# Kernel optimization log

Measured on AMD Instinct MI355X. Metric: run time of the kernel, lower is better.

## Reference

```python
import jax, jax.numpy as jnp
import numpy as np

DIM = 64
NUM_GRAPHS = 512


def setup_inputs() -> dict:
    key = jax.random.key(0)
    ks = jax.random.split(key, 24)
    N, E, F = 20000, 60000, 11
    rn = lambda k, s, sc: jax.random.normal(k, s, jnp.float32) * sc
    return {
        "x": jax.random.normal(ks[0], (N, F), jnp.float32),
        "edge_index": jax.random.randint(ks[1], (2, E), 0, N),
        "edge_attr": jax.random.uniform(ks[2], (E, 5), jnp.float32),
        "batch": jnp.sort(jax.random.randint(ks[3], (N,), 0, NUM_GRAPHS)),
        # lin0: num_features -> dim
        "lin0_w": rn(ks[4], (DIM, F), 0.3), "lin0_b": jnp.zeros(DIM, jnp.float32),
        # edge MLP: 5 -> 128 -> dim*dim
        "nn1_w": rn(ks[5], (128, 5), 0.3), "nn1_b": jnp.zeros(128, jnp.float32),
        "nn2_w": rn(ks[6], (DIM * DIM, 128), 0.02), "nn2_b": jnp.zeros(DIM * DIM, jnp.float32),
        # NNConv root weight + bias
        "root_w": rn(ks[7], (DIM, DIM), 0.1), "conv_b": jnp.zeros(DIM, jnp.float32),
        # GRU (input dim, hidden dim) gates r,z,n
        "gru_w_ih": rn(ks[8], (3 * DIM, DIM), 0.1), "gru_w_hh": rn(ks[9], (3 * DIM, DIM), 0.1),
        "gru_b_ih": jnp.zeros(3 * DIM, jnp.float32), "gru_b_hh": jnp.zeros(3 * DIM, jnp.float32),
        # Set2Set LSTM: input 2*dim, hidden dim, gates i,f,g,o
        "lstm_w_ih": rn(ks[10], (4 * DIM, 2 * DIM), 0.1), "lstm_w_hh": rn(ks[11], (4 * DIM, DIM), 0.1),
        "lstm_b_ih": jnp.zeros(4 * DIM, jnp.float32), "lstm_b_hh": jnp.zeros(4 * DIM, jnp.float32),
        # readout
        "lin1_w": rn(ks[12], (DIM, 2 * DIM), 0.1), "lin1_b": jnp.zeros(DIM, jnp.float32),
        "lin2_w": rn(ks[13], (1, DIM), 0.1), "lin2_b": jnp.zeros(1, jnp.float32),
    }


def reference(x, edge_index, edge_attr, batch,
              lin0_w, lin0_b, nn1_w, nn1_b, nn2_w, nn2_b, root_w, conv_b,
              gru_w_ih, gru_w_hh, gru_b_ih, gru_b_hh,
              lstm_w_ih, lstm_w_hh, lstm_b_ih, lstm_b_hh,
              lin1_w, lin1_b, lin2_w, lin2_b):
    N = x.shape[0]
    src, dst = edge_index[0], edge_index[1]
    # per-edge weight matrices from edge MLP (edge_attr is constant across the 3 conv calls)
    We = (jax.nn.relu(edge_attr @ nn1_w.T + nn1_b) @ nn2_w.T + nn2_b).reshape(-1, DIM, DIM)
    deg = jnp.maximum(jax.ops.segment_sum(jnp.ones_like(src, jnp.float32), dst, N), 1.0)[:, None]

    out = jax.nn.relu(x @ lin0_w.T + lin0_b)
    h = out  # GRU hidden, shape [N, dim]
    for _ in range(3):
        # NNConv: gather src -> per-edge matmul -> scatter-mean at dst, plus root + bias
        msg = jnp.einsum('ei,eio->eo', out[src], We)
        agg = jax.ops.segment_sum(msg, dst, N) / deg
        m = jax.nn.relu(agg + out @ root_w.T + conv_b)
        # single GRU step (PyTorch gate layout r,z,n)
        gi = m @ gru_w_ih.T + gru_b_ih
        gh = h @ gru_w_hh.T + gru_b_hh
        ir, iz, inn = jnp.split(gi, 3, -1)
        hr, hz, hn = jnp.split(gh, 3, -1)
        r = jax.nn.sigmoid(ir + hr)
        z = jax.nn.sigmoid(iz + hz)
        n = jnp.tanh(inn + r * hn)
        h = (1.0 - z) * n + z * h
        out = h

    # Set2Set pooling, 3 processing steps
    B = NUM_GRAPHS
    q_star = jnp.zeros((B, 2 * DIM), out.dtype)
    hs = jnp.zeros((B, DIM), out.dtype)
    cs = jnp.zeros((B, DIM), out.dtype)
    for _ in range(3):
        gates = q_star @ lstm_w_ih.T + lstm_b_ih + hs @ lstm_w_hh.T + lstm_b_hh
        gi, gf, gg, go = jnp.split(gates, 4, -1)
        cs = jax.nn.sigmoid(gf) * cs + jax.nn.sigmoid(gi) * jnp.tanh(gg)
        hs = jax.nn.sigmoid(go) * jnp.tanh(cs)
        q = hs
        e = jnp.sum(out * q[batch], axis=-1)                 # [N]
        emax = jax.ops.segment_max(e, batch, B)
        a = jnp.exp(e - emax[batch])
        a = a / jax.ops.segment_sum(a, batch, B)[batch]      # scatter-softmax
        r_ = jax.ops.segment_sum(a[:, None] * out, batch, B)  # [B, dim]
        q_star = jnp.concatenate([q, r_], axis=-1)

    y = jax.nn.relu(q_star @ lin1_w.T + lin1_b) @ lin2_w.T + lin2_b
    return y.reshape(-1)
```

## Files before the change

### kernel.cpp

```cpp
#include <hip/hip_runtime.h>
#include <math.h>


typedef _Float16 f16x8 __attribute__((ext_vector_type(8)));
typedef _Float16 h2 __attribute__((ext_vector_type(2)));
typedef float f32x4 __attribute__((ext_vector_type(4)));

#define BFRAG_TOTAL (66 * 4 * 4 * 64 * 8)
#define GFRAG_TOTAL (4 * 16 * 64 * 8)
#define PAIRS_CAP 40064
#define PMAX 152
#define SPLITK 4
#define ITERS 8
#define NB_BS 66
#define NB_GS 16
#define NB_H1 (PAIRS_CAP / 128)

#if __has_builtin(__builtin_amdgcn_fdot2)
#define FDOT2(a, b, c) __builtin_amdgcn_fdot2((a), (b), (c), false)
#else
__device__ __forceinline__ float FDOT2(h2 a, h2 b, float c) {
  return c + (float)a[0] * (float)b[0] + (float)a[1] * (float)b[1];
}
#endif

__global__ void k_gc(const int* __restrict__ batch, int* __restrict__ gptr,
                     const int* __restrict__ eidx, int* __restrict__ cnt,
                     int N, int E, int B) {
  int i = blockIdx.x * 256 + threadIdx.x;
  if (i < N) {
    int b = batch[i];
    int bp = (i == 0) ? -1 : batch[i - 1];
    for (int g = bp + 1; g <= b; ++g) gptr[g] = i;
    if (i == N - 1) {
      for (int g = b + 1; g <= B; ++g) gptr[g] = N;
    }
  }
  if (i < E) atomicAdd(&cnt[eidx[E + i]], 1);
}

__global__ __launch_bounds__(1024) void k_scan(const int* __restrict__ cnt,
                                               int* __restrict__ dptr2, int N) {
  __shared__ int wsum[16];
  int t = threadIdx.x;
  int lane = t & 63, wid = t >> 6;
  if (t == 0) dptr2[0] = 0;
  int running = 0;
  for (int base = 0; base < N; base += 1024) {
    int x = (base + t < N) ? ((cnt[base + t] + 1) & ~1) : 0;
#pragma unroll
    for (int d = 1; d < 64; d <<= 1) {
      int u = __shfl_up(x, d, 64);
      if (lane >= d) x += u;
    }
    if (lane == 63) wsum[wid] = x;
    __syncthreads();
    if (wid == 0) {
      int y = (lane < 16) ? wsum[lane] : 0;
#pragma unroll
      for (int d = 1; d < 16; d <<= 1) {
        int u = __shfl_up(y, d, 64);
        if (lane >= d) y += u;
      }
      if (lane < 16) wsum[lane] = y;
    }
    __syncthreads();
    int add = running + (wid > 0 ? wsum[wid - 1] : 0);
    if (base + t < N) dptr2[base + t + 1] = add + x;
    running += wsum[15];
    __syncthreads();
  }
}

__global__ void k_fill(const int* __restrict__ eidx, const int* __restrict__ dptr2,
                       int* __restrict__ fill, int* __restrict__ srcs_s,
                       int* __restrict__ eord, int E) {
  int e = blockIdx.x * 256 + threadIdx.x;
  if (e >= E) return;
  int d = eidx[E + e];
  int pos = dptr2[d] + atomicAdd(&fill[d], 1);
  srcs_s[pos] = eidx[e];
  eord[pos] = e;
}

__global__ __launch_bounds__(256) void k_prep(
    const float* __restrict__ nn2_w, const float* __restrict__ nn2_b,
    const float* __restrict__ root_w, _Float16* __restrict__ Bh,
    _Float16* __restrict__ Bl,
    const float* __restrict__ gw_ih, const float* __restrict__ gw_hh,
    _Float16* __restrict__ Gh, _Float16* __restrict__ Gl,
    const float* __restrict__ eattr, const int* __restrict__ eord,
    const int* __restrict__ eidx, const int* __restrict__ cnt,
    const float* __restrict__ nn1_w, const float* __restrict__ nn1_b,
    f16x8* __restrict__ hp, int E,
    const float* __restrict__ x, const float* __restrict__ lin0_w,
    const float* __restrict__ lin0_b, float* __restrict__ outn, int N) {
  __shared__ float shmem[8192];
  const int bid = blockIdx.x;
  const int t = threadIdx.x;

  if (bid < NB_BS) {
    float* lds = shmem;
    const int kc = bid;
    if (kc < 64) {
      for (int r = t; r < 4096; r += 256) {
        float2 v = *(const float2*)&nn2_w[(size_t)r * 128 + kc * 2];
        lds[r * 2] = v.x;
        lds[r * 2 + 1] = v.y;
      }
    } else if (kc == 64) {
      for (int r = t; r < 4096; r += 256) {
        lds[r * 2] = nn2_b[r];
        lds[r * 2 + 1] = 0.f;
      }
    } else {
      for (int r = t; r < 4096; r += 256) {
        int i = r >> 6, o = r & 63;
        lds[r * 2] = root_w[o * 64 + i];
        lds[r * 2 + 1] = 0.f;
      }
    }
    __syncthreads();
    for (int slot = t; slot < 1024; slot += 256) {
      int lane = slot & 63, c = (slot >> 6) & 3, w = slot >> 8;
      f16x8 ph, pl;
#pragma unroll
      for (int j = 0; j < 8; ++j) {
        int mm = w * 32 + ((lane >> 4) << 3) + j;
        int o = c * 16 + (lane & 15);
        int i = mm & 63, kl = mm >> 6;
        float v = lds[(i * 64 + o) * 2 + kl];
        _Float16 h = (_Float16)v;
        ph[j] = h;
        pl[j] = (_Float16)(v - (float)h);
      }
      size_t base = (((size_t)kc * 4 + w) * 4 + c) * 512 + (size_t)lane * 8;
      *(f16x8*)&Bh[base] = ph;
      *(f16x8*)&Bl[base] = pl;
    }
  } else if (bid < NB_BS + NB_GS) {
    const int c = bid - NB_BS;
    const int w = t >> 6, lane = t & 63;
    const int part = c >> 2, dblk = c & 3;
    f16x8 oh, ol;
#pragma unroll
    for (int j = 0; j < 8; ++j) {
      int k = w * 32 + ((lane >> 4) << 3) + j;
      int d = dblk * 16 + (lane & 15);
      float v;
      if (part == 0) {
        v = (k < 64) ? gw_ih[(size_t)d * 64 + k]
                     : gw_hh[(size_t)d * 64 + (k - 64)];
      } else if (part == 1) {
        v = (k < 64) ? gw_ih[(size_t)(64 + d) * 64 + k]
                     : gw_hh[(size_t)(64 + d) * 64 + (k - 64)];
      } else if (part == 2) {
        v = (k < 64) ? gw_ih[(size_t)(128 + d) * 64 + k] : 0.f;
      } else {
        v = (k >= 64) ? gw_hh[(size_t)(128 + d) * 64 + (k - 64)] : 0.f;
      }
      _Float16 h = (_Float16)v;
      oh[j] = h;
      ol[j] = (_Float16)(v - (float)h);
    }
    size_t base = ((size_t)(w * 16 + c) * 64 + lane) * 8;
    *(f16x8*)&Gh[base] = oh;
    *(f16x8*)&Gl[base] = ol;
  } else if (bid < NB_BS + NB_GS + NB_H1) {
    float* w5 = shmem;
    float* bb = shmem + 640;
    float* at = shmem + 768;
    float* idg = shmem + 2048;
    float* vf1 = shmem + 2176;
    const int m0 = (bid - NB_BS - NB_GS) * 128;
    for (int idx = t; idx < 640; idx += 256) w5[idx] = nn1_w[idx];
    if (t < 128) bb[t] = nn1_b[t];
    if (t < 128) {
      int m = m0 + t;
      int e0 = eord[2 * m], e1 = eord[2 * m + 1];
      float iv = 0.f, vf = 0.f;
      if (e0 >= 0) {
        const float* a = eattr + (size_t)e0 * 5;
#pragma unroll
        for (int q = 0; q < 5; ++q) at[t * 10 + q] = a[q];
        int dg = cnt[eidx[E + e0]];
        iv = 1.f / (float)(dg > 1 ? dg : 1);
        if (e1 >= 0) {
          const float* b = eattr + (size_t)e1 * 5;
#pragma unroll
          for (int q = 0; q < 5; ++q) at[t * 10 + 5 + q] = b[q];
          vf = 1.f;
        } else {
#pragma unroll
          for (int q = 0; q < 5; ++q) at[t * 10 + 5 + q] = 0.f;
        }
      } else {
#pragma unroll
        for (int q = 0; q < 10; ++q) at[t * 10 + q] = 0.f;
      }
      idg[t] = iv;
      vf1[t] = vf;
    }
    __syncthreads();
    const int pl = t & 127, jh = (t >> 7) * 64;
    const int m = m0 + pl;
    float a0 = at[pl * 10 + 0], a1 = at[pl * 10 + 1], a2 = at[pl * 10 + 2],
          a3 = at[pl * 10 + 3], a4 = at[pl * 10 + 4];
    float b0 = at[pl * 10 + 5], b1 = at[pl * 10 + 6], b2 = at[pl * 10 + 7],
          b3 = at[pl * 10 + 8], b4 = at[pl * 10 + 9];
    float iv = idg[pl], vf = vf1[pl];
#pragma unroll 4
    for (int ci = 0; ci < 16; ++ci) {
      int j0 = jh + ci * 4;
      f16x8 o;
#pragma unroll
      for (int u = 0; u < 4; ++u) {
        const float* wr = &w5[(j0 + u) * 5];
        float v0 = fmaxf(bb[j0 + u] + a0 * wr[0] + a1 * wr[1] + a2 * wr[2] +
                             a3 * wr[3] + a4 * wr[4], 0.f) * iv;
        float v1 = fmaxf(bb[j0 + u] + b0 * wr[0] + b1 * wr[1] + b2 * wr[2] +
                             b3 * wr[3] + b4 * wr[4], 0.f) * iv * vf;
        o[2 * u] = (_Float16)v0;
        o[2 * u + 1] = (_Float16)v1;
      }
      hp[(size_t)(j0 >> 2) * PAIRS_CAP + m] = o;
    }
  } else {
    int gid = (bid - NB_BS - NB_GS - NB_H1) * 256 + t;
    int n = gid >> 6, d = gid & 63;
    if (n >= N) return;
    const float* xr = x + (size_t)n * 11;
    const float* wr = lin0_w + d * 11;
    float acc = lin0_b[d];
#pragma unroll
    for (int f = 0; f < 11; ++f) acc += xr[f] * wr[f];
    outn[(size_t)n * 64 + d] = fmaxf(acc, 0.f);
  }
}

__global__ __launch_bounds__(512, 4) void k_fused(
    const float* __restrict__ outn, const f16x8* __restrict__ hp,
    const int* __restrict__ dptr2, const int* __restrict__ cnt,
    const int* __restrict__ srcs_s, const _Float16* __restrict__ Bh,
    const _Float16* __restrict__ Bl, float* __restrict__ agg2, int N) {
  __shared__ __align__(16) _Float16 Ah[32 * 64 * 8];
  __shared__ uint4 sbufq[PMAX * 17];
  __shared__ uint4 hpq[2][PMAX];

  const int t = threadIdx.x;
  const int w = t >> 6, lane = t & 63;
  const int wq = w & 3;
  const int c_off = (w >> 2) * 2;
  const int nl = t >> 3;
  const int io = t & 7;
  const int split = blockIdx.y;
  const int n0 = blockIdx.x * 64;
  const int n = n0 + nl;
  const bool nvalid = (n < N);
  const int hi_n = (n0 + 64 > N) ? N : (n0 + 64);
  const int p0b = dptr2[n0];
  const int p1b = dptr2[hi_n];
  const int MP0 = p0b >> 1;
  const int MPn = (p1b - p0b) >> 1;
  const bool useLds = (MPn <= PMAX);
  int mp0 = 0, mp1 = 0, deg = 0;
  if (nvalid) { mp0 = dptr2[n] >> 1; mp1 = dptr2[n + 1] >> 1; deg = cnt[n]; }
  const float inv = 1.f / (float)(deg > 1 ? deg : 1);
  const int odd = deg & 1;
  const int rt_b = nl >> 4, nm = nl & 15;
  const int MPs = useLds ? MPn : 0;

  for (int idx = t; idx < MPs * 16; idx += 512) {
    int ml = idx >> 4, g = idx & 15;
    int e0s = srcs_s[2 * (MP0 + ml)];
    int e1s = srcs_s[2 * (MP0 + ml) + 1];
    float4 r0 = *(const float4*)(outn + (size_t)e0s * 64 + g * 4);
    float4 r1 = *(const float4*)(outn + (size_t)e1s * 64 + g * 4);
    f16x8 o;
    o[0] = (_Float16)r0.x; o[1] = (_Float16)r1.x;
    o[2] = (_Float16)r0.y; o[3] = (_Float16)r1.y;
    o[4] = (_Float16)r0.z; o[5] = (_Float16)r1.z;
    o[6] = (_Float16)r0.w; o[7] = (_Float16)r1.w;
    sbufq[ml * 17 + (((g >> 2) ^ (ml & 3)) << 2) + (g & 3)] =
        __builtin_bit_cast(uint4, o);
  }
  for (int idx = t; idx < MPs; idx += 512)
    hpq[0][idx] =
        *(const uint4*)&hp[(size_t)(split * ITERS) * PAIRS_CAP + MP0 + idx];
  __syncthreads();

  f32x4 acc[4][2];
#pragma unroll
  for (int a = 0; a < 4; ++a)
#pragma unroll
    for (int c = 0; c < 2; ++c) acc[a][c] = (f32x4)(0.f);

  const int niter = (split == 0) ? (ITERS + 1) : ITERS;
  int cur = 0;
  for (int cc = 0; cc < niter; ++cc) {
    const bool extra = (cc == ITERS);

    float av[4][8];
#pragma unroll
    for (int kl = 0; kl < 4; ++kl)
#pragma unroll
      for (int j = 0; j < 8; ++j) av[kl][j] = 0.f;

    if (!extra) {
      if (useLds) {
        for (int m = mp0; m < mp1; ++m) {
          int ml = m - MP0;
          uint4 hu = hpq[cur][ml];
          h2 h0 = __builtin_bit_cast(h2, hu.x);
          h2 h1 = __builtin_bit_cast(h2, hu.y);
          h2 hh2 = __builtin_bit_cast(h2, hu.z);
          h2 h3 = __builtin_bit_cast(h2, hu.w);
          int sb = ml * 17 + (((io >> 1) ^ (ml & 3)) << 2) + (io & 1) * 2;
          uint4 su0 = sbufq[sb], su1 = sbufq[sb + 1];
          unsigned vs[8] = {su0.x, su0.y, su0.z, su0.w,
                            su1.x, su1.y, su1.z, su1.w};
#pragma unroll
          for (int v = 0; v < 8; ++v) {
            h2 sp = __builtin_bit_cast(h2, vs[v]);
            av[0][v] = FDOT2(h0, sp, av[0][v]);
            av[1][v] = FDOT2(h1, sp, av[1][v]);
            av[2][v] = FDOT2(hh2, sp, av[2][v]);
            av[3][v] = FDOT2(h3, sp, av[3][v]);
          }
        }
      } else {
        const f16x8* hc = hp + (size_t)(split * ITERS + cc) * PAIRS_CAP;
        for (int m = mp0; m < mp1; ++m) {
          f16x8 hv = hc[m];
          int e0s = srcs_s[2 * m], e1s = srcs_s[2 * m + 1];
          const float4* pa = (const float4*)(outn + (size_t)e0s * 64 + io * 8);
          const float4* pb = (const float4*)(outn + (size_t)e1s * 64 + io * 8);
          float4 a0 = pa[0], a1 = pa[1];
          float4 c0 = pb[0], c1 = pb[1];
          float sv0[8] = {a0.x, a0.y, a0.z, a0.w, a1.x, a1.y, a1.z, a1.w};
          float sv1[8] = {c0.x, c0.y, c0.z, c0.w, c1.x, c1.y, c1.z, c1.w};
#pragma unroll
          for (int kl = 0; kl < 4; ++kl) {
            float hA = (float)hv[2 * kl], hB = (float)hv[2 * kl + 1];
#pragma unroll
            for (int j = 0; j < 8; ++j)
              av[kl][j] += hA * sv0[j] + hB * sv1[j];
          }
        }
      }
    } else {
      if (useLds) {
        for (int m = mp0; m < mp1; ++m) {
          int ml = m - MP0;
          h2 msk;
          msk[0] = (_Float16)1.f;
          msk[1] = (_Float16)((odd && m == mp1 - 1) ? 0.f : 1.f);
          int sb = ml * 17 + (((io >> 1) ^ (ml & 3)) << 2) + (io & 1) * 2;
          uint4 su0 = sbufq[sb], su1 = sbufq[sb + 1];
          unsigned vs[8] = {su0.x, su0.y, su0.z, su0.w,
                            su1.x, su1.y, su1.z, su1.w};
#pragma unroll
          for (int v = 0; v < 8; ++v) {
            h2 sp = __builtin_bit_cast(h2, vs[v]);
            av[0][v] = FDOT2(msk, sp, av[0][v]);
          }
        }
      } else {
        for (int m = mp0; m < mp1; ++m) {
          float m1 = (odd && m == mp1 - 1) ? 0.f : 1.f;
          int e0s = srcs_s[2 * m], e1s = srcs_s[2 * m + 1];
          const float4* pa = (const float4*)(outn + (size_t)e0s * 64 + io * 8);
          const float4* pb = (const float4*)(outn + (size_t)e1s * 64 + io * 8);
          float4 a0 = pa[0], a1 = pa[1];
          float4 c0 = pb[0], c1 = pb[1];
          float sv0[8] = {a0.x, a0.y, a0.z, a0.w, a1.x, a1.y, a1.z, a1.w};
          float sv1[8] = {c0.x, c0.y, c0.z, c0.w, c1.x, c1.y, c1.z, c1.w};
#pragma unroll
          for (int j = 0; j < 8; ++j) av[0][j] += sv0[j] + m1 * sv1[j];
        }
      }
#pragma unroll
      for (int j = 0; j < 8; ++j) av[0][j] *= inv;
      if (nvalid) {
        const float4* sp = (const float4*)(outn + (size_t)n * 64 + io * 8);
        float4 s0 = sp[0], s1 = sp[1];
        float sv[8] = {s0.x, s0.y, s0.z, s0.w, s1.x, s1.y, s1.z, s1.w};
#pragma unroll
        for (int j = 0; j < 8; ++j) av[2][j] = sv[j];
      }
    }

#pragma unroll
    for (int kl = 0; kl < 4; ++kl) {
      const int wb = (kl & 1) * 2 + (io >> 2);
      const int q = ((io >> 1) & 1) * 2 + (io & 1);
      const int fb = (kl >> 1) * 16 + wb * 4 + rt_b;
      const int base = (fb * 64 + (q << 4) + nm) * 8;
      f16x8 phv;
#pragma unroll
      for (int jj = 0; jj < 8; ++jj) phv[jj] = (_Float16)av[kl][jj];
      *(f16x8*)&Ah[base] = phv;
    }
    __syncthreads();

#pragma unroll
    for (int ph = 0; ph < 2; ++ph) {
      const int kco = extra ? (64 + ph) : (split * 16 + cc * 2 + ph);
      f16x8 ah[4];
#pragma unroll
      for (int rt = 0; rt < 4; ++rt)
        ah[rt] = *(const f16x8*)&Ah[((ph * 16 + wq * 4 + rt) * 64 + lane) * 8];
      if (ph == 0 && t < 256 && cc + 1 < ITERS) {
        const uint4* hc =
            (const uint4*)&hp[(size_t)(split * ITERS + cc + 1) * PAIRS_CAP + MP0];
        for (int idx = t; idx < MPs; idx += 256) hpq[cur ^ 1][idx] = hc[idx];
      }
      size_t bbase = ((size_t)(kco * 4 + wq) * 4) * 512;
#pragma unroll
      for (int c2 = 0; c2 < 2; ++c2) {
        const int c = c_off + c2;
        f16x8 bh = *(const f16x8*)&Bh[bbase + c * 512 + lane * 8];
        f16x8 bl = *(const f16x8*)&Bl[bbase + c * 512 + lane * 8];
#pragma unroll
        for (int rt = 0; rt < 4; ++rt) {
          acc[rt][c2] = __builtin_amdgcn_mfma_f32_16x16x32_f16(ah[rt], bh, acc[rt][c2], 0, 0, 0);
          acc[rt][c2] = __builtin_amdgcn_mfma_f32_16x16x32_f16(ah[rt], bl, acc[rt][c2], 0, 0, 0);
        }
      }
    }
    __syncthreads();
    if (cc + 1 < ITERS) cur ^= 1;
  }

  {
    float* redb = (float*)Ah;
    const int qrow = (lane >> 4) * 4, col15 = lane & 15;
    const int g14 = ((lane >> 4) & 1) << 4;
    if (wq == 1 || wq == 3) {
      float* L = redb + (wq >> 1) * 4096;
#pragma unroll
      for (int rt = 0; rt < 4; ++rt)
#pragma unroll
        for (int r = 0; r < 4; ++r) {
          int row = rt * 16 + qrow + r;
#pragma unroll
          for (int c2 = 0; c2 < 2; ++c2) {
            int col = (c_off + c2) * 16 + col15;
            L[row * 64 + (col ^ g14)] = acc[rt][c2][r];
          }
        }
    }
    __syncthreads();
    if (wq == 0 || wq == 2) {
      const float* L = redb + (wq >> 1) * 4096;
#pragma unroll
      for (int rt = 0; rt < 4; ++rt)
#pragma unroll
        for (int r = 0; r < 4; ++r) {
          int row = rt * 16 + qrow + r;
#pragma unroll
          for (int c2 = 0; c2 < 2; ++c2) {
            int col = (c_off + c2) * 16 + col15;
            acc[rt][c2][r] += L[row * 64 + (col ^ g14)];
          }
        }
    }
    __syncthreads();
    if (wq == 2) {
      float* L = redb;
#pragma unroll
      for (int rt = 0; rt < 4; ++rt)
#pragma unroll
        for (int r = 0; r < 4; ++r) {
          int row = rt * 16 + qrow + r;
#pragma unroll
          for (int c2 = 0; c2 < 2; ++c2) {
            int col = (c_off + c2) * 16 + col15;
            L[row * 64 + (col ^ g14)] = acc[rt][c2][r];
          }
        }
    }
    __syncthreads();
    if (wq == 0) {
      const float* L = redb;
      float* ag = agg2 + (size_t)split * (size_t)N * 64;
#pragma unroll
      for (int rt = 0; rt < 4; ++rt)
#pragma unroll
        for (int r = 0; r < 4; ++r) {
          int row = rt * 16 + qrow + r;
          int nn = n0 + row;
          if (nn < N) {
#pragma unroll
            for (int c2 = 0; c2 < 2; ++c2) {
              int col = (c_off + c2) * 16 + col15;
              float v = acc[rt][c2][r] + L[row * 64 + (col ^ g14)];
              ag[(size_t)nn * 64 + col] = v;
            }
          }
        }
    }
  }
}

__global__ __launch_bounds__(512) void k_gru2(
    const float* __restrict__ agg2, const float* __restrict__ conv_b,
    const _Float16* __restrict__ Gh, const _Float16* __restrict__ Gl,
    const float* __restrict__ gb_ih, const float* __restrict__ gb_hh,
    float* __restrict__ outn, int N) {
  __shared__ __align__(16) _Float16 Afrag[16 * 64 * 8];
  __shared__ float bih[192], bhh[192];
  const int t = threadIdx.x;
  const int n0 = blockIdx.x * 64;
  const size_t NN = (size_t)N * 64;
  if (t < 192) { bih[t] = gb_ih[t]; bhh[t] = gb_hh[t]; }

  {
    const int nl = t >> 3, io = t & 7;
    const int n = n0 + nl;
    float v[16];
    if (n < N) {
      if (io < 4) {
        const int d0 = io * 16;
        const size_t base = (size_t)n * 64 + d0;
#pragma unroll
        for (int q = 0; q < 4; ++q) {
          float4 s0 = *(const float4*)&agg2[base + q * 4];
          float4 s1 = *(const float4*)&agg2[NN + base + q * 4];
          float4 s2 = *(const float4*)&agg2[2 * NN + base + q * 4];
          float4 s3 = *(const float4*)&agg2[3 * NN + base + q * 4];
          float4 cb = *(const float4*)&conv_b[d0 + q * 4];
          v[q * 4 + 0] = fmaxf(s0.x + s1.x + s2.x + s3.x + cb.x, 0.f);
          v[q * 4 + 1] = fmaxf(s0.y + s1.y + s2.y + s3.y + cb.y, 0.f);
          v[q * 4 + 2] = fmaxf(s0.z + s1.z + s2.z + s3.z + cb.z, 0.f);
          v[q * 4 + 3] = fmaxf(s0.w + s1.w + s2.w + s3.w + cb.w, 0.f);
        }
      } else {
        const int d0 = (io - 4) * 16;
#pragma unroll
        for (int q = 0; q < 4; ++q) {
          float4 h4 = *(const float4*)&outn[(size_t)n * 64 + d0 + q * 4];
          v[q * 4 + 0] = h4.x;
          v[q * 4 + 1] = h4.y;
          v[q * 4 + 2] = h4.z;
          v[q * 4 + 3] = h4.w;
        }
      }
    } else {
#pragma unroll
      for (int j = 0; j < 16; ++j) v[j] = 0.f;
    }
    const int rt = nl >> 4, m = nl & 15;
#pragma unroll
    for (int g2 = 0; g2 < 2; ++g2) {
      int k0 = io * 16 + g2 * 8;
      int ksub = k0 >> 5, kgrp = (k0 >> 3) & 3;
      f16x8 o;
#pragma unroll
      for (int jj = 0; jj < 8; ++jj) o[jj] = (_Float16)v[g2 * 8 + jj];
      *(f16x8*)&Afrag[((ksub * 4 + rt) * 64 + (kgrp << 4) + m) * 8] = o;
    }
  }
  __syncthreads();

  const int w = t >> 6, lane = t & 63;
  const int rt = w >> 1, q2 = (w & 1) * 2;
  f32x4 acc[8];
#pragma unroll
  for (int i = 0; i < 8; ++i) acc[i] = (f32x4)(0.f);
#pragma unroll
  for (int ks = 0; ks < 4; ++ks) {
    f16x8 ah = *(const f16x8*)&Afrag[((ks * 4 + rt) * 64 + lane) * 8];
#pragma unroll
    for (int idx = 0; idx < 8; ++idx) {
      int c = (idx >> 1) * 4 + q2 + (idx & 1);
      f16x8 gh = *(const f16x8*)&Gh[((size_t)(ks * 16 + c) * 64 + lane) * 8];
      f16x8 gl = *(const f16x8*)&Gl[((size_t)(ks * 16 + c) * 64 + lane) * 8];
      acc[idx] = __builtin_amdgcn_mfma_f32_16x16x32_f16(ah, gh, acc[idx], 0, 0, 0);
      acc[idx] = __builtin_amdgcn_mfma_f32_16x16x32_f16(ah, gl, acc[idx], 0, 0, 0);
    }
  }
  const int qrow = (lane >> 4) * 4, col = lane & 15;
#pragma unroll
  for (int c01 = 0; c01 < 2; ++c01) {
    const int d = (q2 + c01) * 16 + col;
#pragma unroll
    for (int r = 0; r < 4; ++r) {
      const int n = n0 + rt * 16 + qrow + r;
      if (n < N) {
        float rs = acc[c01][r], zs = acc[2 + c01][r];
        float inn = acc[4 + c01][r], hn = acc[6 + c01][r];
        float h = outn[(size_t)n * 64 + d];
        float rg = 1.f / (1.f + expf(-(rs + bih[d] + bhh[d])));
        float zg = 1.f / (1.f + expf(-(zs + bih[64 + d] + bhh[64 + d])));
        float ng = tanhf(inn + bih[128 + d] + rg * (hn + bhh[128 + d]));
        outn[(size_t)n * 64 + d] = (1.f - zg) * ng + zg * h;
      }
    }
  }
}

__global__ __launch_bounds__(256) void k_s2s(
    const float* __restrict__ outn, const int* __restrict__ gptr,
    const float* __restrict__ w_ih, const float* __restrict__ w_hh,
    const float* __restrict__ b_ih, const float* __restrict__ b_hh,
    const float* __restrict__ w1, const float* __restrict__ b1,
    const float* __restrict__ w2, const float* __restrict__ b2,
    float* __restrict__ y) {
  __shared__ float q[128];
  __shared__ float hsL[64];
  __shared__ float csL[64];
  __shared__ float gate[256];
  __shared__ float red[4][66];
  const int b = blockIdx.x, t = threadIdx.x;
  const int wv = t >> 6, d = t & 63;
  const int n0 = gptr[b], n1 = gptr[b + 1];
  if (t < 128) q[t] = 0.f;
  if (t < 64) { hsL[t] = 0.f; csL[t] = 0.f; }
  __syncthreads();

  for (int step = 0; step < 3; ++step) {
    float acc = b_ih[t] + b_hh[t];
    const float* wi = w_ih + t * 128;
    const float* wh = w_hh + t * 64;
#pragma unroll 4
    for (int k = 0; k < 128; ++k) acc += wi[k] * q[k];
#pragma unroll 4
    for (int k = 0; k < 64; ++k) acc += wh[k] * hsL[k];
    gate[t] = acc;
    __syncthreads();
    if (t < 64) {
      float ig = gate[t], fg = gate[64 + t], gg = gate[128 + t],
            og = gate[192 + t];
      float c = csL[t];
      float si = 1.f / (1.f + expf(-ig));
      float sf = 1.f / (1.f + expf(-fg));
      float so = 1.f / (1.f + expf(-og));
      float cn = sf * c + si * tanhf(gg);
      csL[t] = cn;
      hsL[t] = so * tanhf(cn);
    }
    __syncthreads();

    float qd = hsL[d];
    float mx = -3.4e38f, den = 0.f, racc = 0.f;
    for (int nn = n0 + wv; nn < n1; nn += 4) {
      float od = outn[(size_t)nn * 64 + d];
      float v = od * qd;
      for (int s = 32; s > 0; s >>= 1) v += __shfl_xor(v, s);
      float mnew = fmaxf(mx, v);
      float scale = expf(mx - mnew);
      float a = expf(v - mnew);
      den = den * scale + a;
      racc = racc * scale + a * od;
      mx = mnew;
    }
    if (d == 0) { red[wv][0] = mx; red[wv][1] = den; }
    red[wv][2 + d] = racc;
    __syncthreads();
    if (t < 64) {
      float M = fmaxf(fmaxf(red[0][0], red[1][0]), fmaxf(red[2][0], red[3][0]));
      float dd = 0.f, rr = 0.f;
#pragma unroll
      for (int ww = 0; ww < 4; ++ww) {
        float sc = expf(red[ww][0] - M);
        dd += red[ww][1] * sc;
        rr += red[ww][2 + t] * sc;
      }
      float r = (dd > 0.f) ? rr / dd : 0.f;
      q[t] = hsL[t];
      q[64 + t] = r;
    }
    __syncthreads();
  }

  if (t < 64) {
    float acc = b1[t];
    const float* wr = w1 + t * 128;
#pragma unroll 4
    for (int k = 0; k < 128; ++k) acc += wr[k] * q[k];
    acc = fmaxf(acc, 0.f) * w2[t];
    for (int s = 32; s > 0; s >>= 1) acc += __shfl_xor(acc, s);
    if (t == 0) y[b] = acc + b2[0];
  }
}

extern "C" void kernel_launch(void* const* d_in, const int* in_sizes, int n_in,
                              void* d_out, int out_size, void* d_ws,
                              size_t ws_size, hipStream_t stream) {
  (void)n_in; (void)out_size; (void)ws_size;
  const float* x      = (const float*)d_in[0];
  const int*   eidx   = (const int*)d_in[1];
  const float* eattr  = (const float*)d_in[2];
  const int*   batch  = (const int*)d_in[3];
  const float* lin0_w = (const float*)d_in[4];
  const float* lin0_b = (const float*)d_in[5];
  const float* nn1_w  = (const float*)d_in[6];
  const float* nn1_b  = (const float*)d_in[7];
  const float* nn2_w  = (const float*)d_in[8];
  const float* nn2_b  = (const float*)d_in[9];
  const float* root_w = (const float*)d_in[10];
  const float* conv_b = (const float*)d_in[11];
  const float* gw_ih  = (const float*)d_in[12];
  const float* gw_hh  = (const float*)d_in[13];
  const float* gb_ih  = (const float*)d_in[14];
  const float* gb_hh  = (const float*)d_in[15];
  const float* lw_ih  = (const float*)d_in[16];
  const float* lw_hh  = (const float*)d_in[17];
  const float* lb_ih  = (const float*)d_in[18];
  const float* lb_hh  = (const float*)d_in[19];
  const float* lin1_w = (const float*)d_in[20];
  const float* lin1_b = (const float*)d_in[21];
  const float* lin2_w = (const float*)d_in[22];
  const float* lin2_b = (const float*)d_in[23];

  const int N = in_sizes[0] / 11;
  const int E = in_sizes[1] / 2;
  const int B = 512;

  size_t off = 0;
  auto bump = [&](size_t bytes) {
    size_t o = off;
    off += (bytes + 255) & ~(size_t)255;
    return o;
  };
  char* base = (char*)d_ws;
  float*     outn   = (float*)(base + bump((size_t)N * 64 * 4));
  float*     agg2   = (float*)(base + bump((size_t)SPLITK * N * 64 * 4));
  f16x8*     hpG    = (f16x8*)(base + bump((size_t)32 * PAIRS_CAP * 16));
  _Float16*  Bh     = (_Float16*)(base + bump((size_t)BFRAG_TOTAL * 2));
  _Float16*  Bl     = (_Float16*)(base + bump((size_t)BFRAG_TOTAL * 2));
  _Float16*  Gh     = (_Float16*)(base + bump((size_t)GFRAG_TOTAL * 2));
  _Float16*  Gl     = (_Float16*)(base + bump((size_t)GFRAG_TOTAL * 2));
  int*       cnt    = (int*)(base + bump((size_t)2 * N * 4));
  int*       fill   = cnt + N;
  int*       dptr2  = (int*)(base + bump((size_t)(N + 1) * 4));
  int*       srcs_s = (int*)(base + bump((size_t)2 * PAIRS_CAP * 4));
  int*       eord   = (int*)(base + bump((size_t)2 * PAIRS_CAP * 4));
  int*       gptr   = (int*)(base + bump((size_t)(B + 1) * 4));

  hipMemsetAsync(cnt, 0, (size_t)2 * N * 4, stream);
  hipMemsetAsync(srcs_s, 0, (size_t)2 * PAIRS_CAP * 4, stream);
  hipMemsetAsync(eord, 0xFF, (size_t)2 * PAIRS_CAP * 4, stream);

  const int gcGrid = ((N > E ? N : E) + 255) / 256;
  k_gc<<<gcGrid, 256, 0, stream>>>(batch, gptr, eidx, cnt, N, E, B);
  k_scan<<<1, 1024, 0, stream>>>(cnt, dptr2, N);
  k_fill<<<(E + 255) / 256, 256, 0, stream>>>(eidx, dptr2, fill, srcs_s, eord, E);

  const int NB_L0 = (N * 64 + 255) / 256;
  k_prep<<<NB_BS + NB_GS + NB_H1 + NB_L0, 256, 0, stream>>>(
      nn2_w, nn2_b, root_w, Bh, Bl, gw_ih, gw_hh, Gh, Gl, eattr, eord, eidx,
      cnt, nn1_w, nn1_b, hpG, E, x, lin0_w, lin0_b, outn, N);

  const int NBLK = (N + 63) / 64;
  for (int it = 0; it < 3; ++it) {
    k_fused<<<dim3(NBLK, SPLITK), 512, 0, stream>>>(outn, hpG, dptr2, cnt,
                                                    srcs_s, Bh, Bl, agg2, N);
    k_gru2<<<NBLK, 512, 0, stream>>>(agg2, conv_b, Gh, Gl, gb_ih, gb_hh, outn,
                                     N);
  }

  k_s2s<<<B, 256, 0, stream>>>(outn, gptr, lw_ih, lw_hh, lb_ih, lb_hh, lin1_w,
                               lin1_b, lin2_w, lin2_b, (float*)d_out);
}
```

Before: 616.1 us.

## Split fused MFMA work across K-phase per wave group instead of output columns

Each wave group now handles one K-phase (ph) across all four output column tiles, instead of both K-phases for two column tiles. Each wave loads its A fragments once per iteration rather than twice, at the cost of doubling the accumulator registers (16 f32x4). The cross-wave reduction becomes a deeper tree that uses the sbufq LDS region as extra scratch, and all 512 threads now prefetch hp. The larger register footprint may lower occupancy under launch_bounds(512,4).

```diff
diff --git a/kernel.cpp b/kernel.cpp
--- a/kernel.cpp
+++ b/kernel.cpp
@@ -249,8 +249,8 @@
 
   const int t = threadIdx.x;
   const int w = t >> 6, lane = t & 63;
+  const int phw = w >> 2;
   const int wq = w & 3;
-  const int c_off = (w >> 2) * 2;
   const int nl = t >> 3;
   const int io = t & 7;
   const int split = blockIdx.y;
@@ -289,11 +289,11 @@
         *(const uint4*)&hp[(size_t)(split * ITERS) * PAIRS_CAP + MP0 + idx];
   __syncthreads();
 
-  f32x4 acc[4][2];
+  f32x4 acc[4][4];
 #pragma unroll
   for (int a = 0; a < 4; ++a)
 #pragma unroll
-    for (int c = 0; c < 2; ++c) acc[a][c] = (f32x4)(0.f);
+    for (int c = 0; c < 4; ++c) acc[a][c] = (f32x4)(0.f);
 
   const int niter = (split == 0) ? (ITERS + 1) : ITERS;
   int cur = 0;
@@ -403,28 +403,26 @@
     }
     __syncthreads();
 
-#pragma unroll
-    for (int ph = 0; ph < 2; ++ph) {
-      const int kco = extra ? (64 + ph) : (split * 16 + cc * 2 + ph);
+    {
+      const int kco = extra ? (64 + phw) : (split * 16 + cc * 2 + phw);
       f16x8 ah[4];
 #pragma unroll
       for (int rt = 0; rt < 4; ++rt)
-        ah[rt] = *(const f16x8*)&Ah[((ph * 16 + wq * 4 + rt) * 64 + lane) * 8];
-      if (ph == 0 && t < 256 && cc + 1 < ITERS) {
+        ah[rt] = *(const f16x8*)&Ah[((phw * 16 + wq * 4 + rt) * 64 + lane) * 8];
+      if (cc + 1 < ITERS) {
         const uint4* hc =
             (const uint4*)&hp[(size_t)(split * ITERS + cc + 1) * PAIRS_CAP + MP0];
-        for (int idx = t; idx < MPs; idx += 256) hpq[cur ^ 1][idx] = hc[idx];
+        for (int idx = t; idx < MPs; idx += 512) hpq[cur ^ 1][idx] = hc[idx];
       }
       size_t bbase = ((size_t)(kco * 4 + wq) * 4) * 512;
 #pragma unroll
-      for (int c2 = 0; c2 < 2; ++c2) {
-        const int c = c_off + c2;
+      for (int c = 0; c < 4; ++c) {
         f16x8 bh = *(const f16x8*)&Bh[bbase + c * 512 + lane * 8];
         f16x8 bl = *(const f16x8*)&Bl[bbase + c * 512 + lane * 8];
 #pragma unroll
         for (int rt = 0; rt < 4; ++rt) {
-          acc[rt][c2] = __builtin_amdgcn_mfma_f32_16x16x32_f16(ah[rt], bh, acc[rt][c2], 0, 0, 0);
-          acc[rt][c2] = __builtin_amdgcn_mfma_f32_16x16x32_f16(ah[rt], bl, acc[rt][c2], 0, 0, 0);
+          acc[rt][c] = __builtin_amdgcn_mfma_f32_16x16x32_f16(ah[rt], bh, acc[rt][c], 0, 0, 0);
+          acc[rt][c] = __builtin_amdgcn_mfma_f32_16x16x32_f16(ah[rt], bl, acc[rt][c], 0, 0, 0);
         }
       }
     }
@@ -433,56 +431,76 @@
   }
 
   {
-    float* redb = (float*)Ah;
+    float* sA = (float*)Ah;
+    float* sB = (float*)sbufq;
     const int qrow = (lane >> 4) * 4, col15 = lane & 15;
     const int g14 = ((lane >> 4) & 1) << 4;
-    if (wq == 1 || wq == 3) {
-      float* L = redb + (wq >> 1) * 4096;
+    if (phw == 1) {
+      float* L = (wq < 2) ? (sA + wq * 4096) : (sB + (wq - 2) * 4096);
 #pragma unroll
       for (int rt = 0; rt < 4; ++rt)
 #pragma unroll
         for (int r = 0; r < 4; ++r) {
           int row = rt * 16 + qrow + r;
 #pragma unroll
-          for (int c2 = 0; c2 < 2; ++c2) {
-            int col = (c_off + c2) * 16 + col15;
-            L[row * 64 + (col ^ g14)] = acc[rt][c2][r];
-          }
-        }
-    }
-    __syncthreads();
-    if (wq == 0 || wq == 2) {
-      const float* L = redb + (wq >> 1) * 4096;
+          for (int c = 0; c < 4; ++c)
+            L[row * 64 + ((c * 16 + col15) ^ g14)] = acc[rt][c][r];
+        }
+    }
+    __syncthreads();
+    if (phw == 0) {
+      const float* L = (wq < 2) ? (sA + wq * 4096) : (sB + (wq - 2) * 4096);
 #pragma unroll
       for (int rt = 0; rt < 4; ++rt)
 #pragma unroll
         for (int r = 0; r < 4; ++r) {
           int row = rt * 16 + qrow + r;
 #pragma unroll
-          for (int c2 = 0; c2 < 2; ++c2) {
-            int col = (c_off + c2) * 16 + col15;
-            acc[rt][c2][r] += L[row * 64 + (col ^ g14)];
-          }
-        }
-    }
-    __syncthreads();
-    if (wq == 2) {
-      float* L = redb;
+          for (int c = 0; c < 4; ++c)
+            acc[rt][c][r] += L[row * 64 + ((c * 16 + col15) ^ g14)];
+        }
+    }
+    __syncthreads();
+    if (phw == 0 && (wq & 1)) {
+      float* L = sA + (wq >> 1) * 4096;
 #pragma unroll
       for (int rt = 0; rt < 4; ++rt)
 #pragma unroll
         for (int r = 0; r < 4; ++r) {
           int row = rt * 16 + qrow + r;
 #pragma unroll
-          for (int c2 = 0; c2 < 2; ++c2) {
-            int col = (c_off + c2) * 16 + col15;
-            L[row * 64 + (col ^ g14)] = acc[rt][c2][r];
+          for (int c = 0; c < 4; ++c)
+            L[row * 64 + ((c * 16 + col15) ^ g14)] = acc[rt][c][r];
+        }
+    }
+    __syncthreads();
+    if (phw == 0 && !(wq & 1)) {
+      const float* L = sA + (wq >> 1) * 4096;
+#pragma unroll
+      for (int rt = 0; rt < 4; ++rt)
+#pragma unroll
+        for (int r = 0; r < 4; ++r) {
+          int row = rt * 16 + qrow + r;
+#pragma unroll
+          for (int c = 0; c < 4; ++c)
+            acc[rt][c][r] += L[row * 64 + ((c * 16 + col15) ^ g14)];
+        }
+      if (wq == 2) {
+        float* L2 = sB;
+#pragma unroll
+        for (int rt = 0; rt < 4; ++rt)
+#pragma unroll
+          for (int r = 0; r < 4; ++r) {
+            int row = rt * 16 + qrow + r;
+#pragma unroll
+            for (int c = 0; c < 4; ++c)
+              L2[row * 64 + ((c * 16 + col15) ^ g14)] = acc[rt][c][r];
           }
-        }
-    }
-    __syncthreads();
-    if (wq == 0) {
-      const float* L = redb;
+      }
+    }
+    __syncthreads();
+    if (phw == 0 && wq == 0) {
+      const float* L = sB;
       float* ag = agg2 + (size_t)split * (size_t)N * 64;
 #pragma unroll
       for (int rt = 0; rt < 4; ++rt)
@@ -492,10 +510,9 @@
           int nn = n0 + row;
           if (nn < N) {
 #pragma unroll
-            for (int c2 = 0; c2 < 2; ++c2) {
-              int col = (c_off + c2) * 16 + col15;
-              float v = acc[rt][c2][r] + L[row * 64 + (col ^ g14)];
-              ag[(size_t)nn * 64 + col] = v;
+            for (int c = 0; c < 4; ++c) {
+              float v = acc[rt][c][r] + L[row * 64 + ((c * 16 + col15) ^ g14)];
+              ag[(size_t)nn * 64 + c * 16 + col15] = v;
             }
           }
         }
```

Result: no change. 616.9 us (+0.1%).
